# Optimization experiments

Hardware: AMD Instinct MI355X
Metric: run time of the kernel (lower is better)

Reference implementation:

```python
import jax, jax.numpy as jnp
import numpy as np

GRID = 128      # voxel grid extent per axis
NUM_BATCH = 4
N_PER = 25000   # points per scene (unique voxels)
C = 128
K = 32          # number of classes in probs
HEADS = 8
SCALE = 1.0


def setup_inputs() -> dict:
    key = jax.random.key(0)
    ks = jax.random.split(key, 12)
    N = NUM_BATCH * N_PER
    # unique voxel coordinates per scene (submanifold conv assumes no duplicate sites)
    coords_list = []
    for b in range(NUM_BATCH):
        flat = jax.random.permutation(jax.random.fold_in(ks[0], b), GRID ** 3)[:N_PER]
        xyz = jnp.stack([flat // (GRID * GRID), (flat // GRID) % GRID, flat % GRID], axis=1)
        bcol = jnp.full((N_PER, 1), b)
        coords_list.append(jnp.concatenate([bcol, xyz], axis=1))
    coords = jnp.concatenate(coords_list, axis=0).astype(jnp.int32)  # [N,4] = (b,x,y,z)
    feats = jax.random.normal(ks[1], (N, C), jnp.float32)
    probs = jax.random.normal(ks[2], (N, K), jnp.float32)
    conv_w = jax.random.normal(ks[3], (27, C, C), jnp.float32) * (1.0 / np.sqrt(27 * C))
    bn_gamma = 1.0 + 0.1 * jax.random.normal(ks[4], (C,), jnp.float32)
    bn_beta = 0.1 * jax.random.normal(ks[5], (C,), jnp.float32)
    in_proj_w = jax.random.normal(ks[6], (3 * C, C), jnp.float32) / np.sqrt(C)
    in_proj_b = 0.01 * jax.random.normal(ks[7], (3 * C,), jnp.float32)
    out_proj_w = jax.random.normal(ks[8], (C, C), jnp.float32) / np.sqrt(C)
    out_proj_b = 0.01 * jax.random.normal(ks[9], (C,), jnp.float32)
    bottleneck_w = jax.random.normal(ks[10], (C, 2 * C), jnp.float32) / np.sqrt(2 * C)
    return {"feats": feats, "probs": probs, "conv_w": conv_w, "bn_gamma": bn_gamma,
            "bn_beta": bn_beta, "in_proj_w": in_proj_w, "in_proj_b": in_proj_b,
            "out_proj_w": out_proj_w, "out_proj_b": out_proj_b,
            "bottleneck_w": bottleneck_w, "coords": coords, "batch_size": NUM_BATCH}


def _subm_conv3x3(feats, coords, conv_w, batch_size):
    """Submanifold 3x3x3 sparse conv: outputs only at active sites, gathering active neighbors."""
    N = feats.shape[0]
    b, xyz = coords[:, 0], coords[:, 1:]
    grid = jnp.full((batch_size, GRID, GRID, GRID), -1, jnp.int32)
    grid = grid.at[b, xyz[:, 0], xyz[:, 1], xyz[:, 2]].set(jnp.arange(N, dtype=jnp.int32))
    out = jnp.zeros((N, conv_w.shape[-1]), feats.dtype)
    kidx = 0
    for dx in (-1, 0, 1):
        for dy in (-1, 0, 1):
            for dz in (-1, 0, 1):
                nb = xyz + jnp.array([dx, dy, dz], jnp.int32)
                inb = jnp.all((nb >= 0) & (nb < GRID), axis=1)
                nbc = jnp.clip(nb, 0, GRID - 1)
                j = grid[b, nbc[:, 0], nbc[:, 1], nbc[:, 2]]
                ok = inb & (j >= 0)
                g = jnp.where(ok[:, None], feats[jnp.maximum(j, 0)], 0.0)
                out = out + g @ conv_w[kidx]
                kidx += 1
    return out


def _forward(feats, probs, conv_w, bn_gamma, bn_beta, in_proj_w, in_proj_b,
             out_proj_w, out_proj_b, bottleneck_w, coords, batch_size):
    N, Cc = feats.shape
    dh = Cc // HEADS
    b = coords[:, 0]
    # transform_input: SubMConv3d -> BatchNorm1d (batch stats) -> ReLU
    x = _subm_conv3x3(feats, coords, conv_w, batch_size)
    mu = jnp.mean(x, axis=0)
    var = jnp.var(x, axis=0)
    x = jax.nn.relu((x - mu) * jax.lax.rsqrt(var + 1e-5) * bn_gamma + bn_beta)
    # SpatialGatherModule: per-scene softmax over points, soft-weighted context [B,K,C]
    m = b[None, :] == jnp.arange(batch_size, dtype=b.dtype)[:, None]          # [B,N]
    neg = jnp.finfo(x.dtype).min
    z = jnp.where(m[:, :, None], (SCALE * probs)[None], neg)                  # [B,N,K]
    w = jax.nn.softmax(z, axis=1)
    ctx = jnp.einsum('bnk,nc->bkc', w, x)                                     # [B,K,C]
    # per-scene MultiheadAttention (unbatched): query = points, key/value = context
    Wq, Wk, Wv = in_proj_w[:Cc], in_proj_w[Cc:2 * Cc], in_proj_w[2 * Cc:]
    bq, bk, bv = in_proj_b[:Cc], in_proj_b[Cc:2 * Cc], in_proj_b[2 * Cc:]
    q = ((x @ Wq.T + bq) * (dh ** -0.5)).reshape(N, HEADS, dh)
    kh = (ctx @ Wk.T + bk).reshape(batch_size, -1, HEADS, dh)
    vh = (ctx @ Wv.T + bv).reshape(batch_size, -1, HEADS, dh)
    scores = jnp.einsum('nhd,bkhd->nbhk', q, kh)
    scores = scores[jnp.arange(N), b]                                         # [N,H,K] pick own scene
    attn = jax.nn.softmax(scores, axis=-1)
    o = jnp.einsum('nhk,bkhd->nbhd', attn, vh)[jnp.arange(N), b]              # [N,H,dh]
    attn_out = o.reshape(N, Cc) @ out_proj_w.T + out_proj_b
    # torch code aliases feats with inputs.features, so the in-place scatter makes
    # both halves of the concat equal to attn_out (literal forward semantics)
    y = jnp.concatenate([attn_out, attn_out], axis=1) @ bottleneck_w.T
    return y


def reference(feats, probs, conv_w, bn_gamma, bn_beta, in_proj_w, in_proj_b,
              out_proj_w, out_proj_b, bottleneck_w, coords, batch_size):
    return _forward(feats, probs, conv_w, bn_gamma, bn_beta, in_proj_w, in_proj_b,
                    out_proj_w, out_proj_b, bottleneck_w, coords, batch_size)
```

## Files before the change

### kernel.cpp

```cpp
#include <hip/hip_runtime.h>
#include <hip/hip_bf16.h>

typedef __attribute__((ext_vector_type(8))) short short8;
typedef __attribute__((ext_vector_type(4))) float floatx4;

#define NB 4
#define GRIDD 128
#define GRID3 (128*128*128)
#define C 128
#define KSLOT 32
#define CTX_BPB 128
#define DEN_BLK 256
#define PCAP 8192

static __device__ __forceinline__ unsigned short f2bf(float f){
  unsigned u = __builtin_bit_cast(unsigned, f);
  unsigned r = (u + 0x7FFFu + ((u >> 16) & 1u)) >> 16;
  return (unsigned short)r;
}
static __device__ __forceinline__ float bf2f(unsigned short h){
  unsigned u = ((unsigned)h) << 16;
  return __builtin_bit_cast(float, u);
}

__global__ void prepk(const float* __restrict__ feats, const float* __restrict__ convw,
                      const float* __restrict__ inw,
                      unsigned short* __restrict__ Fb, unsigned short* __restrict__ Wt,
                      unsigned short* __restrict__ Wq, unsigned short* __restrict__ WkvT,
                      long total1)
{
  const long stride = (long)gridDim.x * blockDim.x;
  const long i0 = (long)blockIdx.x * blockDim.x + threadIdx.x;
  const long q4 = total1 >> 2;
  const float4* f4 = reinterpret_cast<const float4*>(feats);
  ushort4* fb4 = reinterpret_cast<ushort4*>(Fb);
  for (long i = i0; i < q4; i += stride){
    const float4 v = f4[i];
    ushort4 o; o.x = f2bf(v.x); o.y = f2bf(v.y); o.z = f2bf(v.z); o.w = f2bf(v.w);
    fb4[i] = o;
  }
  for (long i = i0; i < 27L*C*C; i += stride){
    long k = i >> 14; long r = (i >> 7) & 127; long c = i & 127;
    Wt[i] = f2bf(convw[(k << 14) + (c << 7) + r]);
  }
  for (long i = i0; i < C*C; i += stride) Wq[i] = f2bf(inw[i]);
  for (long i = i0; i < 2L*C*C; i += stride){
    long which = i >> 14, rem = i & 16383, ii = rem >> 7, cout = rem & 127;
    WkvT[i] = f2bf(inw[((1 + which) << 14) + (cout << 7) + ii]);
  }
}

__global__ __launch_bounds__(128) void w2k(const float* __restrict__ bw,
                                           const float* __restrict__ outw,
                                           const float* __restrict__ outb,
                                           unsigned short* __restrict__ W2b,
                                           float* __restrict__ b2){
  const int o = blockIdx.x, i = threadIdx.x;
  __shared__ float wcf[128];
  __shared__ float red[128];
  const float w_i = bw[(size_t)o*256 + i] + bw[(size_t)o*256 + 128 + i];
  wcf[i] = w_i;
  red[i] = w_i * outb[i];
  __syncthreads();
  float acc = 0.f;
  #pragma unroll 8
  for (int j = 0; j < 128; j++) acc = fmaf(wcf[j], outw[j*128 + i], acc);
  W2b[o*128 + i] = f2bf(acc);
  for (int s = 64; s > 0; s >>= 1){
    if (i < s) red[i] += red[i + s];
    __syncthreads();
  }
  if (i == 0) b2[o] = red[0];
}

__global__ void scatterk(const int* __restrict__ coords, int* __restrict__ gh, int N){
  int p = blockIdx.x * 256 + threadIdx.x;
  if (p < N){
    int4 cr = *reinterpret_cast<const int4*>(coords + (size_t)p * 4);
    gh[(((cr.x*GRIDD + cr.y)*GRIDD + cr.z)*GRIDD) + cr.w] = p;
  }
}

__global__ __launch_bounds__(256) void pairk(const int* __restrict__ coords,
                                             const int* __restrict__ gh,
                                             int2* __restrict__ pairs,
                                             int* __restrict__ gcnt, int N){
  __shared__ int lcnt[27], lbase[27];
  const int t = threadIdx.x;
  if (t < 27) lcnt[t] = 0;
  __syncthreads();
  const int p = blockIdx.x * 256 + t;
  const bool active = p < N;
  int jl[27];
  if (active){
    const int4 cr = *reinterpret_cast<const int4*>(coords + (size_t)p * 4);
    const int b = cr.x, x = cr.y, y = cr.z, z = cr.w;
    #pragma unroll
    for (int k = 0; k < 27; k++){
      if (k == 13){ jl[k] = -1; continue; }
      const int dx = k / 9 - 1, dy = (k / 3) % 3 - 1, dz = k % 3 - 1;
      const int nx = x + dx, ny = y + dy, nz = z + dz;
      const bool ok = ((unsigned)nx < 128u) & ((unsigned)ny < 128u) & ((unsigned)nz < 128u);
      const int gi = ((((b << 7) + (nx & 127)) << 7) + (ny & 127)) * GRIDD + (nz & 127);
      const int jj = gh[gi];
      jl[k] = ok ? jj : -1;
      if (jl[k] >= 0) atomicAdd(&lcnt[k], 1);
    }
  }
  __syncthreads();
  if (t < 27 && t != 13 && lcnt[t] > 0) lbase[t] = atomicAdd(&gcnt[t], lcnt[t]);
  __syncthreads();
  if (t < 27) lcnt[t] = 0;
  __syncthreads();
  if (active){
    #pragma unroll
    for (int k = 0; k < 27; k++){
      if (k == 13) continue;
      if (jl[k] >= 0){
        const int slot = lbase[k] + atomicAdd(&lcnt[k], 1);
        if (slot < PCAP) pairs[(size_t)k * PCAP + slot] = make_int2(p, jl[k]);
      }
    }
  }
}

__global__ __launch_bounds__(256) void scatk(
    const unsigned short* __restrict__ F, const unsigned short* __restrict__ Wt,
    const int2* __restrict__ pairs, const int* __restrict__ gcnt,
    float* __restrict__ X, int N)
{
  __shared__ unsigned short wl[128 * 136];
  const int k = (blockIdx.x < 13) ? blockIdx.x : blockIdx.x + 1;
  const int t = threadIdx.x;
  const unsigned short* wg = Wt + (size_t)k * C * C;
  for (int idx = t; idx < 128 * 16; idx += 256){
    const int row = idx >> 4, seg = idx & 15;
    *reinterpret_cast<short8*>(&wl[row * 136 + seg * 8]) =
        *reinterpret_cast<const short8*>(wg + row * 128 + seg * 8);
  }
  __syncthreads();
  const int cnt = min(gcnt[k], PCAP);
  const int nch = (cnt + 15) >> 4;
  const int wave = t >> 6, lane = t & 63, lo = lane & 15, hi = lane >> 4;
  for (int c = blockIdx.y * 4 + wave; c < nch; c += 32 * 4){
    const int pidx = c * 16 + lo;
    const bool pv = pidx < cnt;
    const int2 pr = pv ? pairs[(size_t)k * PCAP + pidx] : make_int2(0, 0);
    const unsigned short* frow = F + (size_t)pr.y * C;
    short8 a[4];
    #pragma unroll
    for (int kc = 0; kc < 4; kc++){
      a[kc] = *reinterpret_cast<const short8*>(frow + kc * 32 + hi * 8);
      if (!pv) a[kc] = (short8){0,0,0,0,0,0,0,0};
    }
    floatx4 acc[8];
    #pragma unroll
    for (int i = 0; i < 8; i++) acc[i] = (floatx4){0.f,0.f,0.f,0.f};
    #pragma unroll
    for (int kc = 0; kc < 4; kc++){
      const int koff = kc * 32 + hi * 8;
      #pragma unroll
      for (int ct = 0; ct < 8; ct++){
        const short8 b = *reinterpret_cast<const short8*>(&wl[(ct*16 + lo) * 136 + koff]);
        acc[ct] = __builtin_amdgcn_mfma_f32_16x16x32_bf16(a[kc], b, acc[ct], 0, 0, 0);
      }
    }
    #pragma unroll
    for (int i2 = 0; i2 < 4; i2++){
      const int src = hi * 4 + i2;
      const int row = __shfl(pr.x, src);
      if (c * 16 + src < cnt){
        #pragma unroll
        for (int ct = 0; ct < 8; ct++)
          atomicAdd(&X[(size_t)row * C + ct * 16 + lo], acc[ct][i2]);
      }
    }
  }
}

__global__ __launch_bounds__(256) void denomk(const float* __restrict__ probs,
                                              const int* __restrict__ coords,
                                              float* __restrict__ dpart,
                                              float* __restrict__ wexp, int N){
  const int t = threadIdx.x, k = t & 31, rh = t >> 5;
  float a0 = 0.f, a1 = 0.f, a2 = 0.f, a3 = 0.f;
  for (int r = blockIdx.x * 8 + rh; r < N; r += DEN_BLK * 8){
    const int b = coords[(size_t)r * 4];
    const float e = __expf(probs[(size_t)r * 32 + k]);
    wexp[(size_t)r * 32 + k] = e;
    a0 += (b == 0) ? e : 0.f;
    a1 += (b == 1) ? e : 0.f;
    a2 += (b == 2) ? e : 0.f;
    a3 += (b == 3) ? e : 0.f;
  }
  __shared__ float ls[8][128];
  ls[rh][0*32 + k] = a0; ls[rh][1*32 + k] = a1;
  ls[rh][2*32 + k] = a2; ls[rh][3*32 + k] = a3;
  __syncthreads();
  if (t < 128){
    float s = 0.f;
    #pragma unroll
    for (int j = 0; j < 8; j++) s += ls[j][t];
    dpart[(size_t)blockIdx.x * 128 + t] = s;
  }
}

__global__ __launch_bounds__(256) void statsk(const float* __restrict__ X,
                                              float* __restrict__ spgs, int N){
  const int t = threadIdx.x, c = t & 127, rh = t >> 7;
  float s = 0.f, s2 = 0.f;
  for (int r = blockIdx.x * 2 + rh; r < N; r += 512){
    const float v = X[(size_t)r * C + c];
    s += v; s2 += v * v;
  }
  __shared__ float ls[256], ls2[256];
  ls[t] = s; ls2[t] = s2;
  __syncthreads();
  spgs[(size_t)blockIdx.x * 256 + t] =
      (t < 128) ? (ls[t] + ls[t + 128]) : (ls2[t - 128] + ls2[t]);
}

__global__ __launch_bounds__(128) void reduk(const float* __restrict__ pgs, int nblk,
                                             const float* __restrict__ dpart,
                                             float* __restrict__ gsum,
                                             float* __restrict__ gsq,
                                             float* __restrict__ denom){
  const int which = blockIdx.x, slice = blockIdx.y, t = threadIdx.x;
  float s = 0.f;
  if (which < 2){
    const float* src = pgs + which * 128 + t;
    for (int j = slice; j < nblk; j += 8) s += src[(size_t)j * 256];
    atomicAdd((which ? gsq : gsum) + t, s);
  } else {
    const float* src = dpart + t;
    for (int j = slice; j < DEN_BLK; j += 8) s += src[(size_t)j * 128];
    atomicAdd(denom + t, s);
  }
}

__global__ void finalizek(const float* __restrict__ sums, const float* __restrict__ sumsq,
                          const float* __restrict__ gamma, const float* __restrict__ beta,
                          const float* __restrict__ denom,
                          float* __restrict__ scalev, float* __restrict__ shiftv,
                          float* __restrict__ invden, int N){
  const int t = threadIdx.x;
  const float invN = 1.f / (float)N;
  const float mu = sums[t] * invN;
  const float var = sumsq[t] * invN - mu * mu;
  const float sc = gamma[t] * rsqrtf(var + 1e-5f);
  scalev[t] = sc;
  shiftv[t] = beta[t] - mu * sc;
  invden[t] = 1.f / denom[t];
}

__global__ __launch_bounds__(256) void ctx2k(const float* __restrict__ Xm,
                                             const float* __restrict__ wexp,
                                             const float* __restrict__ scalev,
                                             const float* __restrict__ shiftv,
                                             float* __restrict__ pbuf, int NPER){
  const int blk = blockIdx.x;
  const int b = blk >> 7, j = blk & 127;
  const int rows = (NPER + CTX_BPB - 1) / CTX_BPB;
  const int r0 = j * rows;
  const int r1 = min(r0 + rows, NPER);
  const int t = threadIdx.x, c = t & 127, rh = t >> 7;
  const float sc = scalev[c], sh = shiftv[c];
  float acc[KSLOT];
  #pragma unroll
  for (int k = 0; k < KSLOT; k++) acc[k] = 0.f;
  for (int r = r0 + rh; r < r1; r += 2){
    const size_t nn = (size_t)b * NPER + r;
    const float xv = fmaxf(fmaf(Xm[nn * C + c], sc, sh), 0.f);
    const float4* wr = reinterpret_cast<const float4*>(wexp + nn * KSLOT);
    #pragma unroll
    for (int kq = 0; kq < 8; kq++){
      const float4 w4 = wr[kq];
      acc[kq*4+0] = fmaf(w4.x, xv, acc[kq*4+0]);
      acc[kq*4+1] = fmaf(w4.y, xv, acc[kq*4+1]);
      acc[kq*4+2] = fmaf(w4.z, xv, acc[kq*4+2]);
      acc[kq*4+3] = fmaf(w4.w, xv, acc[kq*4+3]);
    }
  }
  __shared__ float red[2 * KSLOT * C];
  #pragma unroll
  for (int k = 0; k < KSLOT; k++) red[(rh * KSLOT + k) * C + c] = acc[k];
  __syncthreads();
  float* dst = pbuf + (size_t)blk * KSLOT * C;
  for (int i = t; i < KSLOT * C; i += 256) dst[i] = red[i] + red[KSLOT * C + i];
}

__global__ __launch_bounds__(256) void kvk(const float* __restrict__ pbuf,
                                           const float* __restrict__ invden,
                                           const unsigned short* __restrict__ WkvT,
                                           const float* __restrict__ inb,
                                           float* __restrict__ kh, float* __restrict__ vh){
  __shared__ float rowp[2][C];
  __shared__ float row[C];
  const int bk = blockIdx.x;
  const int b = bk >> 5, k = bk & 31;
  const int t = threadIdx.x, c = t & 127, jh = t >> 7;
  float s = 0.f;
  for (int j = jh; j < CTX_BPB; j += 2)
    s += pbuf[((size_t)(b * CTX_BPB + j) * KSLOT + k) * C + c];
  rowp[jh][c] = s;
  __syncthreads();
  if (t < C) row[t] = (rowp[0][t] + rowp[1][t]) * invden[b * KSLOT + k];
  __syncthreads();
  const int which = t >> 7;
  const unsigned short* W = WkvT + (size_t)which * C * C;
  float acc = inb[(1 + which) * C + c];
  #pragma unroll 8
  for (int i = 0; i < C; i++) acc = fmaf(row[i], bf2f(W[i * C + c]), acc);
  (which ? vh : kh)[(size_t)bk * C + c] = acc;
}

__global__ __launch_bounds__(256) void gemm128(
    const unsigned short* __restrict__ A, const unsigned short* __restrict__ W,
    const float* __restrict__ bias, float scale,
    float* __restrict__ outF, unsigned short* __restrict__ outB, int N)
{
  const int tid = threadIdx.x;
  const int wave = tid >> 6, lane = tid & 63;
  const int rbase = blockIdx.x * 64 + (wave >> 1) * 32;
  const int cbase = (wave & 1) * 64;
  const int lo = lane & 15, hi = lane >> 4;
  floatx4 acc[2][4];
  #pragma unroll
  for (int rt = 0; rt < 2; rt++)
    #pragma unroll
    for (int ct = 0; ct < 4; ct++) acc[rt][ct] = (floatx4){0.f,0.f,0.f,0.f};
  const int m0 = rbase + lo, m1 = rbase + 16 + lo;
  const int m0c = m0 < N ? m0 : N - 1;
  const int m1c = m1 < N ? m1 : N - 1;
  #pragma unroll
  for (int kc = 0; kc < 4; kc++){
    const int koff = kc * 32 + hi * 8;
    const short8 a0 = *reinterpret_cast<const short8*>(A + (size_t)m0c * C + koff);
    const short8 a1 = *reinterpret_cast<const short8*>(A + (size_t)m1c * C + koff);
    #pragma unroll
    for (int ct = 0; ct < 4; ct++){
      const int n = cbase + ct * 16 + lo;
      const short8 b = *reinterpret_cast<const short8*>(W + (size_t)n * C + koff);
      acc[0][ct] = __builtin_amdgcn_mfma_f32_16x16x32_bf16(a0, b, acc[0][ct], 0, 0, 0);
      acc[1][ct] = __builtin_amdgcn_mfma_f32_16x16x32_bf16(a1, b, acc[1][ct], 0, 0, 0);
    }
  }
  #pragma unroll
  for (int rt = 0; rt < 2; rt++){
    #pragma unroll
    for (int ct = 0; ct < 4; ct++){
      const int col = cbase + ct * 16 + lo;
      const float bv = bias ? bias[col] : 0.f;
      #pragma unroll
      for (int i = 0; i < 4; i++){
        const int row = rbase + rt * 16 + hi * 4 + i;
        if (row < N){
          const float v = (acc[rt][ct][i] + bv) * scale;
          if (outF) outF[(size_t)row * C + col] = v;
          if (outB) outB[(size_t)row * C + col] = f2bf(v);
        }
      }
    }
  }
}

__global__ __launch_bounds__(256) void gemm128f(
    const float* __restrict__ A, const unsigned short* __restrict__ W,
    const float* __restrict__ bias, const float* __restrict__ bnsc,
    const float* __restrict__ bnsh, float scale,
    unsigned short* __restrict__ outB, int N)
{
  const int tid = threadIdx.x;
  const int wave = tid >> 6, lane = tid & 63;
  const int rbase = blockIdx.x * 64 + (wave >> 1) * 32;
  const int cbase = (wave & 1) * 64;
  const int lo = lane & 15, hi = lane >> 4;
  floatx4 acc[2][4];
  #pragma unroll
  for (int rt = 0; rt < 2; rt++)
    #pragma unroll
    for (int ct = 0; ct < 4; ct++) acc[rt][ct] = (floatx4){0.f,0.f,0.f,0.f};
  const int m0 = rbase + lo, m1 = rbase + 16 + lo;
  const int m0c = m0 < N ? m0 : N - 1;
  const int m1c = m1 < N ? m1 : N - 1;
  #pragma unroll
  for (int kc = 0; kc < 4; kc++){
    const int koff = kc * 32 + hi * 8;
    const float4 sc0 = *reinterpret_cast<const float4*>(bnsc + koff);
    const float4 sc1 = *reinterpret_cast<const float4*>(bnsc + koff + 4);
    const float4 sh0 = *reinterpret_cast<const float4*>(bnsh + koff);
    const float4 sh1 = *reinterpret_cast<const float4*>(bnsh + koff + 4);
    const float4 xa0 = *reinterpret_cast<const float4*>(A + (size_t)m0c * C + koff);
    const float4 xa1 = *reinterpret_cast<const float4*>(A + (size_t)m0c * C + koff + 4);
    const float4 xb0 = *reinterpret_cast<const float4*>(A + (size_t)m1c * C + koff);
    const float4 xb1 = *reinterpret_cast<const float4*>(A + (size_t)m1c * C + koff + 4);
    short8 a0, a1;
    const float* sc = &sc0.x; const float* sh = &sh0.x;
    const float* x0 = &xa0.x; const float* x1 = &xb0.x;
    #pragma unroll
    for (int j = 0; j < 4; j++){
      a0[j] = (short)f2bf(fmaxf(fmaf(x0[j], sc[j], sh[j]), 0.f));
      a1[j] = (short)f2bf(fmaxf(fmaf(x1[j], sc[j], sh[j]), 0.f));
    }
    const float* sc2 = &sc1.x; const float* sh2 = &sh1.x;
    const float* x02 = &xa1.x; const float* x12 = &xb1.x;
    #pragma unroll
    for (int j = 0; j < 4; j++){
      a0[4+j] = (short)f2bf(fmaxf(fmaf(x02[j], sc2[j], sh2[j]), 0.f));
      a1[4+j] = (short)f2bf(fmaxf(fmaf(x12[j], sc2[j], sh2[j]), 0.f));
    }
    #pragma unroll
    for (int ct = 0; ct < 4; ct++){
      const int n = cbase + ct * 16 + lo;
      const short8 b = *reinterpret_cast<const short8*>(W + (size_t)n * C + koff);
      acc[0][ct] = __builtin_amdgcn_mfma_f32_16x16x32_bf16(a0, b, acc[0][ct], 0, 0, 0);
      acc[1][ct] = __builtin_amdgcn_mfma_f32_16x16x32_bf16(a1, b, acc[1][ct], 0, 0, 0);
    }
  }
  #pragma unroll
  for (int rt = 0; rt < 2; rt++){
    #pragma unroll
    for (int ct = 0; ct < 4; ct++){
      const int col = cbase + ct * 16 + lo;
      const float bv = bias[col];
      #pragma unroll
      for (int i = 0; i < 4; i++){
        const int row = rbase + rt * 16 + hi * 4 + i;
        if (row < N) outB[(size_t)row * C + col] = f2bf((acc[rt][ct][i] + bv) * scale);
      }
    }
  }
}

__global__ __launch_bounds__(256) void attn3k(const unsigned short* __restrict__ qb,
                                              const float* __restrict__ kh,
                                              const float* __restrict__ vh,
                                              unsigned short* __restrict__ ob, int NPER){
  __shared__ float khL[KSLOT * C];
  __shared__ float vhL[KSLOT * C];
  const int t = threadIdx.x;
  const int b = blockIdx.y;
  const int n0 = blockIdx.x * 32;
  {
    const float4* ks = reinterpret_cast<const float4*>(kh + (size_t)b * KSLOT * C);
    const float4* vs = reinterpret_cast<const float4*>(vh + (size_t)b * KSLOT * C);
    float4* kd = reinterpret_cast<float4*>(khL);
    float4* vd = reinterpret_cast<float4*>(vhL);
    #pragma unroll
    for (int i = 0; i < 4; i++){ kd[i * 256 + t] = ks[i * 256 + t]; vd[i * 256 + t] = vs[i * 256 + t]; }
  }
  __syncthreads();
  const int h = t >> 5, p = t & 31;
  const int n = n0 + p;
  const int nc = n < NPER ? n : NPER - 1;
  float qv[16];
  {
    const short8* qp = reinterpret_cast<const short8*>(qb + ((size_t)b * NPER + nc) * C + h * 16);
    const short8 qa = qp[0], qc = qp[1];
    #pragma unroll
    for (int i = 0; i < 8; i++){
      qv[i]     = bf2f((unsigned short)qa[i]);
      qv[8 + i] = bf2f((unsigned short)qc[i]);
    }
  }
  float sv[KSLOT];
  #pragma unroll
  for (int k = 0; k < KSLOT; k++){
    const float4* kp = reinterpret_cast<const float4*>(&khL[k * C + h * 16]);
    const float4 k0 = kp[0], k1 = kp[1], k2 = kp[2], k3 = kp[3];
    float s;
    s = qv[0] * k0.x;
    s = fmaf(qv[1], k0.y, s);  s = fmaf(qv[2],  k0.z, s);  s = fmaf(qv[3],  k0.w, s);
    s = fmaf(qv[4], k1.x, s);  s = fmaf(qv[5],  k1.y, s);  s = fmaf(qv[6],  k1.z, s);
    s = fmaf(qv[7], k1.w, s);  s = fmaf(qv[8],  k2.x, s);  s = fmaf(qv[9],  k2.y, s);
    s = fmaf(qv[10], k2.z, s); s = fmaf(qv[11], k2.w, s);  s = fmaf(qv[12], k3.x, s);
    s = fmaf(qv[13], k3.y, s); s = fmaf(qv[14], k3.z, s);  s = fmaf(qv[15], k3.w, s);
    sv[k] = s;
  }
  float m = sv[0];
  #pragma unroll
  for (int k = 1; k < KSLOT; k++) m = fmaxf(m, sv[k]);
  float sum = 0.f;
  #pragma unroll
  for (int k = 0; k < KSLOT; k++){ const float e = __expf(sv[k] - m); sv[k] = e; sum += e; }
  const float inv = 1.f / sum;
  float o[16];
  #pragma unroll
  for (int i = 0; i < 16; i++) o[i] = 0.f;
  #pragma unroll
  for (int k = 0; k < KSLOT; k++){
    const float w = sv[k];
    const float4* vp = reinterpret_cast<const float4*>(&vhL[k * C + h * 16]);
    const float4 v0 = vp[0], v1 = vp[1], v2 = vp[2], v3 = vp[3];
    o[0]  = fmaf(w, v0.x, o[0]);  o[1]  = fmaf(w, v0.y, o[1]);
    o[2]  = fmaf(w, v0.z, o[2]);  o[3]  = fmaf(w, v0.w, o[3]);
    o[4]  = fmaf(w, v1.x, o[4]);  o[5]  = fmaf(w, v1.y, o[5]);
    o[6]  = fmaf(w, v1.z, o[6]);  o[7]  = fmaf(w, v1.w, o[7]);
    o[8]  = fmaf(w, v2.x, o[8]);  o[9]  = fmaf(w, v2.y, o[9]);
    o[10] = fmaf(w, v2.z, o[10]); o[11] = fmaf(w, v2.w, o[11]);
    o[12] = fmaf(w, v3.x, o[12]); o[13] = fmaf(w, v3.y, o[13]);
    o[14] = fmaf(w, v3.z, o[14]); o[15] = fmaf(w, v3.w, o[15]);
  }
  if (n < NPER){
    short8 s0, s1;
    #pragma unroll
    for (int i = 0; i < 8; i++){
      s0[i] = (short)f2bf(o[i] * inv);
      s1[i] = (short)f2bf(o[8 + i] * inv);
    }
    unsigned short* op = ob + ((size_t)b * NPER + n) * C + h * 16;
    *reinterpret_cast<short8*>(op) = s0;
    *reinterpret_cast<short8*>(op + 8) = s1;
  }
}

extern "C" void kernel_launch(void* const* d_in, const int* in_sizes, int n_in,
                              void* d_out, int out_size, void* d_ws, size_t ws_size,
                              hipStream_t stream){
  const float* feats  = (const float*)d_in[0];
  const float* probs  = (const float*)d_in[1];
  const float* convw  = (const float*)d_in[2];
  const float* gamma  = (const float*)d_in[3];
  const float* beta   = (const float*)d_in[4];
  const float* inw    = (const float*)d_in[5];
  const float* inb    = (const float*)d_in[6];
  const float* outw   = (const float*)d_in[7];
  const float* outb   = (const float*)d_in[8];
  const float* bw     = (const float*)d_in[9];
  const int*   coords = (const int*)d_in[10];
  const int N = in_sizes[0] / C;
  const int NPER = N / NB;
  const int NBLK = (N + 63) / 64;

  char* ws = (char*)d_ws;
  size_t off = 0;
  auto alloc = [&](size_t bytes) -> char* {
    char* r = ws + off; off += (bytes + 255) & ~(size_t)255; return r;
  };
  int* grid_h            = (int*)alloc((size_t)NB * GRID3 * 4);
  unsigned short* featsb = (unsigned short*)alloc((size_t)N * C * 2);
  unsigned short* convwt = (unsigned short*)alloc((size_t)27 * C * C * 2);
  unsigned short* wq     = (unsigned short*)alloc((size_t)C * C * 2);
  unsigned short* wkvT   = (unsigned short*)alloc((size_t)2 * C * C * 2);
  unsigned short* w2b    = (unsigned short*)alloc((size_t)C * C * 2);
  float* b2              = (float*)alloc(512);
  float* xconv           = (float*)alloc((size_t)N * C * 4);
  int2* pairs            = (int2*)alloc((size_t)27 * PCAP * 8);
  float* spgs            = (float*)alloc((size_t)256 * 256 * 4);
  float* dpart           = (float*)alloc((size_t)DEN_BLK * 128 * 4);
  float* zero_base       = (float*)alloc((size_t)512 * 4);
  float* gsum   = zero_base;
  float* gsq    = zero_base + 128;
  float* denom  = zero_base + 256;
  int*   gcnt   = (int*)(zero_base + 384);
  float* invden = (float*)alloc(512);
  float* scalev = (float*)alloc(512);
  float* shiftv = (float*)alloc(512);
  float* kh     = (float*)alloc((size_t)NB * KSLOT * C * 4);
  float* vh     = (float*)alloc((size_t)NB * KSLOT * C * 4);
  float* wexp = (float*)grid_h;
  float* pbuf = wexp + (size_t)N * KSLOT;
  unsigned short* qb   = (unsigned short*)(pbuf + (size_t)NB * CTX_BPB * KSLOT * C);
  unsigned short* o_bf = featsb;

  const long total1 = (long)N * C;
  (void)hipMemsetAsync(grid_h, 0xFF, (size_t)NB * GRID3 * 4, stream);
  (void)hipMemsetAsync(zero_base, 0, (size_t)512 * 4, stream);
  prepk<<<2048, 256, 0, stream>>>(feats, convw, inw, featsb, convwt, wq, wkvT, total1);
  w2k<<<128, 128, 0, stream>>>(bw, outw, outb, w2b, b2);
  scatterk<<<(N + 255) / 256, 256, 0, stream>>>(coords, grid_h, N);
  pairk<<<(N + 255) / 256, 256, 0, stream>>>(coords, grid_h, pairs, gcnt, N);
  denomk<<<DEN_BLK, 256, 0, stream>>>(probs, coords, dpart, wexp, N);
  gemm128<<<NBLK, 256, 0, stream>>>(featsb, convwt + 13 * C * C, nullptr, 1.f, xconv, nullptr, N);
  scatk<<<dim3(26, 32), 256, 0, stream>>>(featsb, convwt, pairs, gcnt, xconv, N);
  statsk<<<256, 256, 0, stream>>>(xconv, spgs, N);
  {
    dim3 rg(3, 8);
    reduk<<<rg, 128, 0, stream>>>(spgs, 256, dpart, gsum, gsq, denom);
  }
  finalizek<<<1, 128, 0, stream>>>(gsum, gsq, gamma, beta, denom, scalev, shiftv, invden, N);
  ctx2k<<<NB * CTX_BPB, 256, 0, stream>>>(xconv, wexp, scalev, shiftv, pbuf, NPER);
  kvk<<<NB * KSLOT, 256, 0, stream>>>(pbuf, invden, wkvT, inb, kh, vh);
  gemm128f<<<NBLK, 256, 0, stream>>>(xconv, wq, inb, scalev, shiftv, 0.25f, qb, N);
  dim3 agrid((NPER + 31) / 32, NB);
  attn3k<<<agrid, 256, 0, stream>>>(qb, kh, vh, o_bf, NPER);
  gemm128<<<NBLK, 256, 0, stream>>>(o_bf, w2b, b2, 1.f, (float*)d_out, nullptr, N);
}
```

Measured before the change: 486.9 us.

## Skip grid memset via coord verification, ballot-based pair compaction, wider stats reduction

Removes the large memset of the dense voxel hash grid. Stale entries are instead rejected by bounds-checking the index and comparing the neighbor's stored coordinates. Pair compaction now uses wave ballots and popcounts in place of shared-memory atomics. The stats kernel reads float4 vectors across more blocks, the denominator and ctx kernels get more blocks, and qb moves to its own allocation. The main saving is the 32MB memset, at the cost of an extra coordinate gather per neighbor and reliance on uninitialized workspace contents.

```diff
diff --git a/kernel.cpp b/kernel.cpp
--- a/kernel.cpp
+++ b/kernel.cpp
@@ -9,8 +9,9 @@
 #define GRID3 (128*128*128)
 #define C 128
 #define KSLOT 32
-#define CTX_BPB 128
-#define DEN_BLK 256
+#define CTX_BPB 256
+#define DEN_BLK 1024
+#define STAT_BLK 1024
 #define PCAP 8192
 
 static __device__ __forceinline__ unsigned short f2bf(float f){
@@ -85,41 +86,57 @@
                                              const int* __restrict__ gh,
                                              int2* __restrict__ pairs,
                                              int* __restrict__ gcnt, int N){
-  __shared__ int lcnt[27], lbase[27];
-  const int t = threadIdx.x;
-  if (t < 27) lcnt[t] = 0;
-  __syncthreads();
+  __shared__ int wcnt[4][27];
+  __shared__ int woff[4][27];
+  const int t = threadIdx.x, wave = t >> 6, lane = t & 63;
   const int p = blockIdx.x * 256 + t;
   const bool active = p < N;
+  int4 cr = make_int4(0, 0, 0, 0);
+  if (active) cr = *reinterpret_cast<const int4*>(coords + (size_t)p * 4);
+  const int b = cr.x, x = cr.y, y = cr.z, z = cr.w;
   int jl[27];
-  if (active){
-    const int4 cr = *reinterpret_cast<const int4*>(coords + (size_t)p * 4);
-    const int b = cr.x, x = cr.y, y = cr.z, z = cr.w;
-    #pragma unroll
-    for (int k = 0; k < 27; k++){
-      if (k == 13){ jl[k] = -1; continue; }
+  #pragma unroll
+  for (int k = 0; k < 27; k++){
+    jl[k] = -1;
+    if (k == 13) continue;
+    if (active){
       const int dx = k / 9 - 1, dy = (k / 3) % 3 - 1, dz = k % 3 - 1;
       const int nx = x + dx, ny = y + dy, nz = z + dz;
-      const bool ok = ((unsigned)nx < 128u) & ((unsigned)ny < 128u) & ((unsigned)nz < 128u);
-      const int gi = ((((b << 7) + (nx & 127)) << 7) + (ny & 127)) * GRIDD + (nz & 127);
-      const int jj = gh[gi];
-      jl[k] = ok ? jj : -1;
-      if (jl[k] >= 0) atomicAdd(&lcnt[k], 1);
-    }
-  }
-  __syncthreads();
-  if (t < 27 && t != 13 && lcnt[t] > 0) lbase[t] = atomicAdd(&gcnt[t], lcnt[t]);
-  __syncthreads();
-  if (t < 27) lcnt[t] = 0;
-  __syncthreads();
-  if (active){
-    #pragma unroll
-    for (int k = 0; k < 27; k++){
-      if (k == 13) continue;
-      if (jl[k] >= 0){
-        const int slot = lbase[k] + atomicAdd(&lcnt[k], 1);
-        if (slot < PCAP) pairs[(size_t)k * PCAP + slot] = make_int2(p, jl[k]);
+      if (((unsigned)nx < 128u) & ((unsigned)ny < 128u) & ((unsigned)nz < 128u)){
+        const int gi = ((((b << 7) + nx) << 7) + ny) * GRIDD + nz;
+        const int jj = gh[gi];
+        if ((unsigned)jj < (unsigned)N){
+          const int4 cj = *reinterpret_cast<const int4*>(coords + (size_t)jj * 4);
+          if (cj.x == b && cj.y == nx && cj.z == ny && cj.w == nz) jl[k] = jj;
+        }
       }
+    }
+  }
+  #pragma unroll
+  for (int k = 0; k < 27; k++){
+    const unsigned long long m = __ballot(jl[k] >= 0);
+    if (lane == 0) wcnt[wave][k] = (int)__popcll(m);
+  }
+  __syncthreads();
+  if (t < 27){
+    const int c0 = wcnt[0][t], c1 = wcnt[1][t], c2 = wcnt[2][t], c3 = wcnt[3][t];
+    const int tot = c0 + c1 + c2 + c3;
+    int gb = 0;
+    if (t != 13 && tot > 0) gb = atomicAdd(&gcnt[t], tot);
+    woff[0][t] = gb;
+    woff[1][t] = gb + c0;
+    woff[2][t] = gb + c0 + c1;
+    woff[3][t] = gb + c0 + c1 + c2;
+  }
+  __syncthreads();
+  const unsigned long long ltm = ((unsigned long long)1 << lane) - 1;
+  #pragma unroll
+  for (int k = 0; k < 27; k++){
+    if (k == 13) continue;
+    const unsigned long long m = __ballot(jl[k] >= 0);
+    if (jl[k] >= 0){
+      const int slot = woff[wave][k] + (int)__popcll(m & ltm);
+      if (slot < PCAP) pairs[(size_t)k * PCAP + slot] = make_int2(p, jl[k]);
     }
   }
 }
@@ -207,20 +224,34 @@
 
 __global__ __launch_bounds__(256) void statsk(const float* __restrict__ X,
                                               float* __restrict__ spgs, int N){
-  const int t = threadIdx.x, c = t & 127, rh = t >> 7;
-  float s = 0.f, s2 = 0.f;
-  for (int r = blockIdx.x * 2 + rh; r < N; r += 512){
-    const float v = X[(size_t)r * C + c];
-    s += v; s2 += v * v;
-  }
-  __shared__ float ls[256], ls2[256];
-  ls[t] = s; ls2[t] = s2;
-  __syncthreads();
-  spgs[(size_t)blockIdx.x * 256 + t] =
-      (t < 128) ? (ls[t] + ls[t + 128]) : (ls2[t - 128] + ls2[t]);
-}
-
-__global__ __launch_bounds__(128) void reduk(const float* __restrict__ pgs, int nblk,
+  const int t = threadIdx.x, c4 = t & 31, rg = t >> 5;
+  float s0=0.f,s1=0.f,s2=0.f,s3=0.f, q0=0.f,q1=0.f,q2=0.f,q3=0.f;
+  for (int r = blockIdx.x * 8 + rg; r < N; r += STAT_BLK * 8){
+    const float4 v = *reinterpret_cast<const float4*>(X + (size_t)r * C + c4 * 4);
+    s0 += v.x; s1 += v.y; s2 += v.z; s3 += v.w;
+    q0 = fmaf(v.x, v.x, q0); q1 = fmaf(v.y, v.y, q1);
+    q2 = fmaf(v.z, v.z, q2); q3 = fmaf(v.w, v.w, q3);
+  }
+  __shared__ float ls[256][4], lq[256][4];
+  ls[t][0]=s0; ls[t][1]=s1; ls[t][2]=s2; ls[t][3]=s3;
+  lq[t][0]=q0; lq[t][1]=q1; lq[t][2]=q2; lq[t][3]=q3;
+  __syncthreads();
+  if (t < 32){
+    float as[4]={0.f,0.f,0.f,0.f}, aq[4]={0.f,0.f,0.f,0.f};
+    #pragma unroll
+    for (int g = 0; g < 8; g++){
+      #pragma unroll
+      for (int j = 0; j < 4; j++){ as[j] += ls[g*32 + t][j]; aq[j] += lq[g*32 + t][j]; }
+    }
+    #pragma unroll
+    for (int j = 0; j < 4; j++){
+      spgs[(size_t)blockIdx.x * 256 + t*4 + j] = as[j];
+      spgs[(size_t)blockIdx.x * 256 + 128 + t*4 + j] = aq[j];
+    }
+  }
+}
+
+__global__ __launch_bounds__(128) void reduk(const float* __restrict__ pgs,
                                              const float* __restrict__ dpart,
                                              float* __restrict__ gsum,
                                              float* __restrict__ gsq,
@@ -229,7 +260,7 @@
   float s = 0.f;
   if (which < 2){
     const float* src = pgs + which * 128 + t;
-    for (int j = slice; j < nblk; j += 8) s += src[(size_t)j * 256];
+    for (int j = slice; j < STAT_BLK; j += 8) s += src[(size_t)j * 256];
     atomicAdd((which ? gsq : gsum) + t, s);
   } else {
     const float* src = dpart + t;
@@ -259,7 +290,7 @@
                                              const float* __restrict__ shiftv,
                                              float* __restrict__ pbuf, int NPER){
   const int blk = blockIdx.x;
-  const int b = blk >> 7, j = blk & 127;
+  const int b = blk >> 8, j = blk & 255;
   const int rows = (NPER + CTX_BPB - 1) / CTX_BPB;
   const int r0 = j * rows;
   const int r1 = min(r0 + rows, NPER);
@@ -386,28 +417,20 @@
   #pragma unroll
   for (int kc = 0; kc < 4; kc++){
     const int koff = kc * 32 + hi * 8;
-    const float4 sc0 = *reinterpret_cast<const float4*>(bnsc + koff);
-    const float4 sc1 = *reinterpret_cast<const float4*>(bnsc + koff + 4);
-    const float4 sh0 = *reinterpret_cast<const float4*>(bnsh + koff);
-    const float4 sh1 = *reinterpret_cast<const float4*>(bnsh + koff + 4);
-    const float4 xa0 = *reinterpret_cast<const float4*>(A + (size_t)m0c * C + koff);
-    const float4 xa1 = *reinterpret_cast<const float4*>(A + (size_t)m0c * C + koff + 4);
-    const float4 xb0 = *reinterpret_cast<const float4*>(A + (size_t)m1c * C + koff);
-    const float4 xb1 = *reinterpret_cast<const float4*>(A + (size_t)m1c * C + koff + 4);
     short8 a0, a1;
-    const float* sc = &sc0.x; const float* sh = &sh0.x;
-    const float* x0 = &xa0.x; const float* x1 = &xb0.x;
-    #pragma unroll
-    for (int j = 0; j < 4; j++){
-      a0[j] = (short)f2bf(fmaxf(fmaf(x0[j], sc[j], sh[j]), 0.f));
-      a1[j] = (short)f2bf(fmaxf(fmaf(x1[j], sc[j], sh[j]), 0.f));
-    }
-    const float* sc2 = &sc1.x; const float* sh2 = &sh1.x;
-    const float* x02 = &xa1.x; const float* x12 = &xb1.x;
-    #pragma unroll
-    for (int j = 0; j < 4; j++){
-      a0[4+j] = (short)f2bf(fmaxf(fmaf(x02[j], sc2[j], sh2[j]), 0.f));
-      a1[4+j] = (short)f2bf(fmaxf(fmaf(x12[j], sc2[j], sh2[j]), 0.f));
+    #pragma unroll
+    for (int half = 0; half < 2; half++){
+      const float4 sc = *reinterpret_cast<const float4*>(bnsc + koff + half * 4);
+      const float4 sh = *reinterpret_cast<const float4*>(bnsh + koff + half * 4);
+      const float4 x0 = *reinterpret_cast<const float4*>(A + (size_t)m0c * C + koff + half * 4);
+      const float4 x1 = *reinterpret_cast<const float4*>(A + (size_t)m1c * C + koff + half * 4);
+      const float* scp = &sc.x; const float* shp = &sh.x;
+      const float* x0p = &x0.x; const float* x1p = &x1.x;
+      #pragma unroll
+      for (int j = 0; j < 4; j++){
+        a0[half*4 + j] = (short)f2bf(fmaxf(fmaf(x0p[j], scp[j], shp[j]), 0.f));
+        a1[half*4 + j] = (short)f2bf(fmaxf(fmaf(x1p[j], scp[j], shp[j]), 0.f));
+      }
     }
     #pragma unroll
     for (int ct = 0; ct < 4; ct++){
@@ -545,8 +568,9 @@
   unsigned short* w2b    = (unsigned short*)alloc((size_t)C * C * 2);
   float* b2              = (float*)alloc(512);
   float* xconv           = (float*)alloc((size_t)N * C * 4);
+  unsigned short* qb     = (unsigned short*)alloc((size_t)N * C * 2);
   int2* pairs            = (int2*)alloc((size_t)27 * PCAP * 8);
-  float* spgs            = (float*)alloc((size_t)256 * 256 * 4);
+  float* spgs            = (float*)alloc((size_t)STAT_BLK * 256 * 4);
   float* dpart           = (float*)alloc((size_t)DEN_BLK * 128 * 4);
   float* zero_base       = (float*)alloc((size_t)512 * 4);
   float* gsum   = zero_base;
@@ -560,11 +584,9 @@
   float* vh     = (float*)alloc((size_t)NB * KSLOT * C * 4);
   float* wexp = (float*)grid_h;
   float* pbuf = wexp + (size_t)N * KSLOT;
-  unsigned short* qb   = (unsigned short*)(pbuf + (size_t)NB * CTX_BPB * KSLOT * C);
   unsigned short* o_bf = featsb;
 
   const long total1 = (long)N * C;
-  (void)hipMemsetAsync(grid_h, 0xFF, (size_t)NB * GRID3 * 4, stream);
   (void)hipMemsetAsync(zero_base, 0, (size_t)512 * 4, stream);
   prepk<<<2048, 256, 0, stream>>>(feats, convw, inw, featsb, convwt, wq, wkvT, total1);
   w2k<<<128, 128, 0, stream>>>(bw, outw, outb, w2b, b2);
@@ -573,10 +595,10 @@
   denomk<<<DEN_BLK, 256, 0, stream>>>(probs, coords, dpart, wexp, N);
   gemm128<<<NBLK, 256, 0, stream>>>(featsb, convwt + 13 * C * C, nullptr, 1.f, xconv, nullptr, N);
   scatk<<<dim3(26, 32), 256, 0, stream>>>(featsb, convwt, pairs, gcnt, xconv, N);
-  statsk<<<256, 256, 0, stream>>>(xconv, spgs, N);
+  statsk<<<STAT_BLK, 256, 0, stream>>>(xconv, spgs, N);
   {
     dim3 rg(3, 8);
-    reduk<<<rg, 128, 0, stream>>>(spgs, 256, dpart, gsum, gsq, denom);
+    reduk<<<rg, 128, 0, stream>>>(spgs, dpart, gsum, gsq, denom);
   }
   finalizek<<<1, 128, 0, stream>>>(gsum, gsq, gamma, beta, denom, scalev, shiftv, invden, N);
   ctx2k<<<NB * CTX_BPB, 256, 0, stream>>>(xconv, wexp, scalev, shiftv, pbuf, NPER);
```

Result: faster. 473.9 us (-2.7%).
